# Kernel tuning notes

Hardware: AMD Instinct MI355X
Metric: run time of the kernel (lower is better)

The kernel has to match this reference:

```python
import jax, jax.numpy as jnp
import numpy as np

B, CIN, H, W = 32, 128, 64, 64
OUT, KH, KW = 256, 3, 3
NSK, SDIM = 4, 128


def setup_inputs() -> dict:
    key = jax.random.key(0)
    kx, kw_, kb, ks = jax.random.split(key, 4)
    x = jax.random.normal(kx, (B, CIN, H, W), dtype=jnp.float32)
    kval = float(np.sqrt(1.0 / (CIN * KH * KW)))  # groups=1
    weight = jax.random.uniform(kw_, (OUT, CIN, KH, KW), jnp.float32, -kval, kval)
    bias_tensor = jax.random.uniform(kb, (OUT,), jnp.float32, -kval, kval)
    # Rademacher / sketch_dim, shape (n, s, O) == torch's type1_signed_matrices
    signed = (2.0 * jax.random.bernoulli(ks, 0.5, (NSK, SDIM, OUT)).astype(jnp.float32) - 1.0) / SDIM
    # prod = einsum('ijkl,mi->mjkl') per sketch -> (n, s, Cin, kh, kw)
    prod = jnp.einsum('oikl,nso->nsikl', weight, signed)
    # .permute(2,3,1,0).flatten(0,2): (s,Cin,kh,kw) -> (kh,kw,Cin,s) -> (kh*kw*Cin, s)
    type1_sketches = prod.transpose(0, 3, 4, 2, 1).reshape(NSK, KH * KW * CIN, SDIM)
    return {
        "x": x,
        "type1_sketches": type1_sketches,
        "type1_signed_matrices": signed,
        "bias_tensor": bias_tensor,
    }


def reference(x, type1_sketches, type1_signed_matrices, bias_tensor):
    b, _, h1, w1 = x.shape
    h2 = h1 - KH + 1
    w2 = w1 - KW + 1
    # torch unfold: (B, Cin*KH*KW, E), features ordered channel-major (C, kh, kw)
    patches = jax.lax.conv_general_dilated_patches(
        x, filter_shape=(KH, KW), window_strides=(1, 1), padding='VALID'
    )  # (B, Cin*KH*KW, H2, W2)
    patches = patches.reshape(b, CIN * KH * KW, h2 * w2)  # (B, F, E)
    # 'bnfe,nfs->bnse' with the n-expansion folded away
    y = jnp.einsum('bfe,nfs->bnse', patches, type1_sketches)
    z = jnp.einsum('bnse,nso->bnoe', y, type1_signed_matrices)
    z = z.reshape(b, NSK, OUT, h2, w2)
    out = jnp.mean(z, axis=1) + bias_tensor[None, :, None, None]
    return out
```

## Files before the change

kernel.cpp:

```cpp
#include <hip/hip_runtime.h>
#include <hip/hip_bf16.h>
#include <stdint.h>


#define BATCH 32
#define CIN   128
#define HH    64
#define WW    64
#define OUTC  256
#define H2    62
#define W2    62
#define A_TILE 16384
#define WS_A_BYTES (36 * A_TILE)
#define BROWB 16384
#define AMAX  (35 * A_TILE)

typedef __bf16 bf16x8 __attribute__((ext_vector_type(8)));
typedef float  f32x4  __attribute__((ext_vector_type(4)));

typedef unsigned int u32_as1 __attribute__((address_space(1)));
typedef unsigned int u32_as3 __attribute__((address_space(3)));

__device__ __forceinline__ void async_copy16(const void* g, void* l) {
  __builtin_amdgcn_global_load_lds((const u32_as1*)g, (u32_as3*)l, 16, 0, 0);
}

#define FPB 4
__global__ __launch_bounds__(256) void weff_kernel(
    const float* __restrict__ sketches,
    const float* __restrict__ sgn,
    char* __restrict__ wsA)
{
  __shared__ alignas(16) float sk[512 * FPB];
  const int f0 = blockIdx.x * FPB;
  const int t  = threadIdx.x;

  for (int k = 0; k < (512 * FPB) / 256; ++k) {
    int idx = t + k * 256;
    int fi  = idx >> 9;
    int ns  = idx & 511;
    int n   = ns >> 7;
    int s   = ns & 127;
    sk[ns * FPB + fi] = sketches[(n * 1152 + f0 + fi) * 128 + s];
  }
  __syncthreads();

  const int o = t;
  float acc0 = 0.f, acc1 = 0.f, acc2 = 0.f, acc3 = 0.f;
#pragma unroll 8
  for (int ns = 0; ns < 512; ++ns) {
    float sg = sgn[ns * 256 + o];
    f32x4 skv = *(const f32x4*)(&sk[ns * FPB]);
    acc0 += sg * skv[0];
    acc1 += sg * skv[1];
    acc2 += sg * skv[2];
    acc3 += sg * skv[3];
  }

  float accs[FPB] = {acc0, acc1, acc2, acc3};
#pragma unroll
  for (int fi = 0; fi < FPB; ++fi) {
    int f   = f0 + fi;
    int c   = f / 9;
    int tap = f - c * 9;
    int st  = tap * 4 + (c >> 5);
    int kk  = c & 31;
    uint32_t byteoff = (uint32_t)st * A_TILE + (uint32_t)(o >> 4) * 1024
                     + (uint32_t)(((kk >> 3) * 16 + (o & 15)) * 16)
                     + (uint32_t)((kk & 7) * 2);
    *(__hip_bfloat16*)(wsA + byteoff) = __float2bfloat16(accs[fi] * 0.25f);
  }
}

__global__ __launch_bounds__(512, 2) void conv_kernel(
    const float* __restrict__ x,
    const char*  __restrict__ wA,
    const float* __restrict__ bias,
    float* __restrict__ out)
{
  __shared__ alignas(16) char lds[4 * A_TILE + 6 * BROWB];
  char* ldsA = lds;
  char* ldsB = lds + 4 * A_TILE;

  const int bid = blockIdx.x;
  const int swz = (bid & 7) * 64 + (bid >> 3);
  const int b   = swz >> 4;
  const int ig  = swz & 15;
  const int i0  = ig * 4;

  const int t    = threadIdx.x;
  const int lane = t & 63;
  const int w    = t >> 6;
  const int wm   = w >> 2;
  const int we   = w & 3;

  const char* aSrcLane = wA + w * 2048 + lane * 16;

#define STAGE(AOFF, TGT) do {                                              \
    const char* s_ = aSrcLane + (AOFF);                                    \
    char* d_ = ldsA + (TGT) * A_TILE + w * 2048;                           \
    async_copy16(s_,        d_);                                           \
    async_copy16(s_ + 1024, d_ + 1024);                                    \
  } while (0)

  STAGE(0, 0);
  STAGE(A_TILE, 1);
  STAGE(2 * A_TILE, 2);

  {
    const int j  = t & 63;
    const int cq = t >> 6;
    const uint32_t swb = (uint32_t)((j & 7) << 4);
#pragma unroll
    for (int r = 0; r < 6; ++r) {
      int xrow = i0 + r; if (xrow > 63) xrow = 63;
      const float* xr = x + (((size_t)(b * CIN + cq * 16)) * HH + xrow) * WW + j;
      char* lrow = ldsB + r * BROWB + j * 256;
#pragma unroll
      for (int g = 0; g < 2; ++g) {
        bf16x8 pk;
#pragma unroll
        for (int cc = 0; cc < 8; ++cc)
          pk[cc] = (__bf16)xr[(size_t)(g * 8 + cc) * (HH * WW)];
        uint32_t c0b = (uint32_t)(cq * 32 + g * 16);
        *(bf16x8*)(lrow + (c0b ^ swb)) = pk;
      }
    }
  }

  f32x4 acc[8][4];
  const f32x4 zf = {0.f, 0.f, 0.f, 0.f};
#pragma unroll
  for (int mi = 0; mi < 8; ++mi)
#pragma unroll
    for (int ni = 0; ni < 4; ++ni)
      acc[mi][ni] = zf;

  const int ln15  = lane & 15;
  const int khi16 = (lane >> 4) << 4;
  const char* pA = ldsA + wm * 8192 + lane * 16;

#define MKB(COL, PAR) (ldsB + we * BROWB + (COL) * 256                     \
    + (uint32_t)(((((PAR) * 64) | khi16) ^ (((COL) & 7) << 4))))
  const char* pB00 = MKB(ln15 + 0, 0); const char* pB01 = MKB(ln15 + 0, 1);
  const char* pB10 = MKB(ln15 + 1, 0); const char* pB11 = MKB(ln15 + 1, 1);
  const char* pB20 = MKB(ln15 + 2, 0); const char* pB21 = MKB(ln15 + 2, 1);
  const int c30 = (48 + ln15 + 0 > 63) ? 63 : 48 + ln15 + 0;
  const int c31 = (48 + ln15 + 1 > 63) ? 63 : 48 + ln15 + 1;
  const int c32 = (48 + ln15 + 2 > 63) ? 63 : 48 + ln15 + 2;
  const char* pC00 = MKB(c30, 0); const char* pC01 = MKB(c30, 1);
  const char* pC10 = MKB(c31, 0); const char* pC11 = MKB(c31, 1);
  const char* pC20 = MKB(c32, 0); const char* pC21 = MKB(c32, 1);
#undef MKB

  __syncthreads();

  bf16x8 aX0, aX1, aX2, aX3, aY0, aY1, aY2, aY3, b0, b1, b2, b3;

  aX0 = *(const bf16x8*)(pA);
  aX1 = *(const bf16x8*)(pA + 1024);
  aX2 = *(const bf16x8*)(pA + 2048);
  aX3 = *(const bf16x8*)(pA + 3072);
  b0  = *(const bf16x8*)(pB00);
  b1  = *(const bf16x8*)(pB00 + 4096);
  b2  = *(const bf16x8*)(pB00 + 8192);
  b3  = *(const bf16x8*)(pC00);

  uint32_t aoff = 3 * A_TILE;

#define MFMA_ __builtin_amdgcn_mfma_f32_16x16x32_bf16
#define LGKM0 asm volatile("s_waitcnt lgkmcnt(0)" ::: "memory")
#define VM2   asm volatile("s_waitcnt vmcnt(2)" ::: "memory")

#define MFMA16(A0_, A1_, A2_, A3_, M_) do {                                \
    __builtin_amdgcn_s_setprio(1);                                         \
    acc[(M_)+0][0] = MFMA_(A0_, b0, acc[(M_)+0][0], 0, 0, 0);              \
    acc[(M_)+0][1] = MFMA_(A0_, b1, acc[(M_)+0][1], 0, 0, 0);              \
    acc[(M_)+0][2] = MFMA_(A0_, b2, acc[(M_)+0][2], 0, 0, 0);              \
    acc[(M_)+0][3] = MFMA_(A0_, b3, acc[(M_)+0][3], 0, 0, 0);              \
    acc[(M_)+1][0] = MFMA_(A1_, b0, acc[(M_)+1][0], 0, 0, 0);              \
    acc[(M_)+1][1] = MFMA_(A1_, b1, acc[(M_)+1][1], 0, 0, 0);              \
    acc[(M_)+1][2] = MFMA_(A1_, b2, acc[(M_)+1][2], 0, 0, 0);              \
    acc[(M_)+1][3] = MFMA_(A1_, b3, acc[(M_)+1][3], 0, 0, 0);              \
    acc[(M_)+2][0] = MFMA_(A2_, b0, acc[(M_)+2][0], 0, 0, 0);              \
    acc[(M_)+2][1] = MFMA_(A2_, b1, acc[(M_)+2][1], 0, 0, 0);              \
    acc[(M_)+2][2] = MFMA_(A2_, b2, acc[(M_)+2][2], 0, 0, 0);              \
    acc[(M_)+2][3] = MFMA_(A2_, b3, acc[(M_)+2][3], 0, 0, 0);              \
    acc[(M_)+3][0] = MFMA_(A3_, b0, acc[(M_)+3][0], 0, 0, 0);              \
    acc[(M_)+3][1] = MFMA_(A3_, b1, acc[(M_)+3][1], 0, 0, 0);              \
    acc[(M_)+3][2] = MFMA_(A3_, b2, acc[(M_)+3][2], 0, 0, 0);              \
    acc[(M_)+3][3] = MFMA_(A3_, b3, acc[(M_)+3][3], 0, 0, 0);              \
    __builtin_amdgcn_s_setprio(0);                                         \
  } while (0)

#define STEPQ(Q, KWN, PARN, CK2N) do {                                     \
    VM2;                                                                   \
    __builtin_amdgcn_s_barrier();                                          \
    STAGE(aoff, (Q + 3) & 3);                                              \
    aoff += A_TILE; if (aoff > AMAX) aoff = AMAX;                          \
    LGKM0;                                                                 \
    MFMA16(aX0, aX1, aX2, aX3, 0);                                         \
    aY0 = *(const bf16x8*)(pA + (Q & 3) * A_TILE + 4096);                  \
    aY1 = *(const bf16x8*)(pA + (Q & 3) * A_TILE + 5120);                  \
    aY2 = *(const bf16x8*)(pA + (Q & 3) * A_TILE + 6144);                  \
    aY3 = *(const bf16x8*)(pA + (Q & 3) * A_TILE + 7168);                  \
    __builtin_amdgcn_s_barrier();                                          \
    LGKM0;                                                                 \
    MFMA16(aY0, aY1, aY2, aY3, 4);                                         \
    aX0 = *(const bf16x8*)(pA + ((Q + 1) & 3) * A_TILE);                   \
    aX1 = *(const bf16x8*)(pA + ((Q + 1) & 3) * A_TILE + 1024);            \
    aX2 = *(const bf16x8*)(pA + ((Q + 1) & 3) * A_TILE + 2048);            \
    aX3 = *(const bf16x8*)(pA + ((Q + 1) & 3) * A_TILE + 3072);            \
    b0 = *(const bf16x8*)(pB##KWN##PARN + (CK2N) * 128);                   \
    b1 = *(const bf16x8*)(pB##KWN##PARN + (CK2N) * 128 + 4096);            \
    b2 = *(const bf16x8*)(pB##KWN##PARN + (CK2N) * 128 + 8192);            \
    b3 = *(const bf16x8*)(pC##KWN##PARN + (CK2N) * 128);                   \
  } while (0)

#pragma unroll 1
  for (int kh = 0; kh < 3; ++kh) {
    STEPQ(0, 0, 1, 0);
    STEPQ(1, 0, 0, 1);
    STEPQ(2, 0, 1, 1);
    STEPQ(3, 1, 0, 0);
    STEPQ(4, 1, 1, 0);
    STEPQ(5, 1, 0, 1);
    STEPQ(6, 1, 1, 1);
    STEPQ(7, 2, 0, 0);
    STEPQ(8, 2, 1, 0);
    STEPQ(9, 2, 0, 1);
    STEPQ(10, 2, 1, 1);
    {
      VM2;
      __builtin_amdgcn_s_barrier();
      STAGE(aoff, (11 + 3) & 3);
      aoff += A_TILE; if (aoff > AMAX) aoff = AMAX;
      LGKM0;
      MFMA16(aX0, aX1, aX2, aX3, 0);
      aY0 = *(const bf16x8*)(pA + (11 & 3) * A_TILE + 4096);
      aY1 = *(const bf16x8*)(pA + (11 & 3) * A_TILE + 5120);
      aY2 = *(const bf16x8*)(pA + (11 & 3) * A_TILE + 6144);
      aY3 = *(const bf16x8*)(pA + (11 & 3) * A_TILE + 7168);
      __builtin_amdgcn_s_barrier();
      LGKM0;
      MFMA16(aY0, aY1, aY2, aY3, 4);
      if (kh < 2) {
        pB00 += BROWB; pB01 += BROWB; pB10 += BROWB; pB11 += BROWB;
        pB20 += BROWB; pB21 += BROWB; pC00 += BROWB; pC01 += BROWB;
        pC10 += BROWB; pC11 += BROWB; pC20 += BROWB; pC21 += BROWB;
      }
      aX0 = *(const bf16x8*)(pA);
      aX1 = *(const bf16x8*)(pA + 1024);
      aX2 = *(const bf16x8*)(pA + 2048);
      aX3 = *(const bf16x8*)(pA + 3072);
      b0 = *(const bf16x8*)(pB00);
      b1 = *(const bf16x8*)(pB00 + 4096);
      b2 = *(const bf16x8*)(pB00 + 8192);
      b3 = *(const bf16x8*)(pC00);
    }
  }

#undef STEPQ
#undef MFMA16
#undef VM2
#undef LGKM0
#undef MFMA_
#undef STAGE

  const int jn   = ln15;
  const int g4   = lane >> 4;
  const int irow = i0 + we;
  if (irow < H2) {
#pragma unroll
    for (int mi = 0; mi < 8; ++mi) {
#pragma unroll
      for (int ni = 0; ni < 4; ++ni) {
        const int jj = (ni << 4) + jn;
        if (jj < W2) {
#pragma unroll
          for (int rr = 0; rr < 4; ++rr) {
            const int o = (wm << 7) + (mi << 4) + (g4 << 2) + rr;
            out[(((size_t)b * OUTC + o) * H2 + irow) * W2 + jj] =
                acc[mi][ni][rr] + bias[o];
          }
        }
      }
    }
  }
}

extern "C" void kernel_launch(void* const* d_in, const int* in_sizes, int n_in,
                              void* d_out, int out_size, void* d_ws, size_t ws_size,
                              hipStream_t stream) {
  const float* x        = (const float*)d_in[0];
  const float* sketches = (const float*)d_in[1];
  const float* sgn      = (const float*)d_in[2];
  const float* bias     = (const float*)d_in[3];
  float* out            = (float*)d_out;
  char* wsA             = (char*)d_ws;

  if (ws_size < (size_t)WS_A_BYTES) return;

  weff_kernel<<<1152 / FPB, 256, 0, stream>>>(sketches, sgn, wsA);
  conv_kernel<<<BATCH * 16, 512, 0, stream>>>(x, wsA, bias, out);
}
```

Measured before the change: 105.3 us.

## Double-buffer B fragments in registers and drop the mid-step barrier

Splits the B operand registers into even and odd sets, so the next step's B fragments are read from LDS while the current step's MFMAs run. It also removes the second s_barrier and the explicit lgkmcnt(0) waits inside each step, leaving the compiler to insert the needed waits, with sched_barrier fences fixing the order of reads and MFMAs. The aim is to hide LDS read latency behind matrix math and cut synchronisation stalls. The cost is extra VGPR pressure, and it depends on the remaining per-step barrier being enough to keep the shared tile safe.

```diff
diff --git a/kernel.cpp b/kernel.cpp
--- a/kernel.cpp
+++ b/kernel.cpp
@@ -155,95 +155,93 @@
 
   __syncthreads();
 
-  bf16x8 aX0, aX1, aX2, aX3, aY0, aY1, aY2, aY3, b0, b1, b2, b3;
+  bf16x8 aX0, aX1, aX2, aX3, aY0, aY1, aY2, aY3;
+  bf16x8 bE0, bE1, bE2, bE3, bO0, bO1, bO2, bO3;
+
+#define READB(BN, KWN, PARN, CK2N) do {                                    \
+    BN##0 = *(const bf16x8*)(pB##KWN##PARN + (CK2N) * 128);                \
+    BN##1 = *(const bf16x8*)(pB##KWN##PARN + (CK2N) * 128 + 4096);         \
+    BN##2 = *(const bf16x8*)(pB##KWN##PARN + (CK2N) * 128 + 8192);         \
+    BN##3 = *(const bf16x8*)(pC##KWN##PARN + (CK2N) * 128);                \
+  } while (0)
 
   aX0 = *(const bf16x8*)(pA);
   aX1 = *(const bf16x8*)(pA + 1024);
   aX2 = *(const bf16x8*)(pA + 2048);
   aX3 = *(const bf16x8*)(pA + 3072);
-  b0  = *(const bf16x8*)(pB00);
-  b1  = *(const bf16x8*)(pB00 + 4096);
-  b2  = *(const bf16x8*)(pB00 + 8192);
-  b3  = *(const bf16x8*)(pC00);
+  READB(bE, 0, 0, 0);
 
   uint32_t aoff = 3 * A_TILE;
 
 #define MFMA_ __builtin_amdgcn_mfma_f32_16x16x32_bf16
-#define LGKM0 asm volatile("s_waitcnt lgkmcnt(0)" ::: "memory")
 #define VM2   asm volatile("s_waitcnt vmcnt(2)" ::: "memory")
-
-#define MFMA16(A0_, A1_, A2_, A3_, M_) do {                                \
+#define SB0   __builtin_amdgcn_sched_barrier(0)
+
+#define MFMA16(A0_, A1_, A2_, A3_, BS, M_) do {                            \
     __builtin_amdgcn_s_setprio(1);                                         \
-    acc[(M_)+0][0] = MFMA_(A0_, b0, acc[(M_)+0][0], 0, 0, 0);              \
-    acc[(M_)+0][1] = MFMA_(A0_, b1, acc[(M_)+0][1], 0, 0, 0);              \
-    acc[(M_)+0][2] = MFMA_(A0_, b2, acc[(M_)+0][2], 0, 0, 0);              \
-    acc[(M_)+0][3] = MFMA_(A0_, b3, acc[(M_)+0][3], 0, 0, 0);              \
-    acc[(M_)+1][0] = MFMA_(A1_, b0, acc[(M_)+1][0], 0, 0, 0);              \
-    acc[(M_)+1][1] = MFMA_(A1_, b1, acc[(M_)+1][1], 0, 0, 0);              \
-    acc[(M_)+1][2] = MFMA_(A1_, b2, acc[(M_)+1][2], 0, 0, 0);              \
-    acc[(M_)+1][3] = MFMA_(A1_, b3, acc[(M_)+1][3], 0, 0, 0);              \
-    acc[(M_)+2][0] = MFMA_(A2_, b0, acc[(M_)+2][0], 0, 0, 0);              \
-    acc[(M_)+2][1] = MFMA_(A2_, b1, acc[(M_)+2][1], 0, 0, 0);              \
-    acc[(M_)+2][2] = MFMA_(A2_, b2, acc[(M_)+2][2], 0, 0, 0);              \
-    acc[(M_)+2][3] = MFMA_(A2_, b3, acc[(M_)+2][3], 0, 0, 0);              \
-    acc[(M_)+3][0] = MFMA_(A3_, b0, acc[(M_)+3][0], 0, 0, 0);              \
-    acc[(M_)+3][1] = MFMA_(A3_, b1, acc[(M_)+3][1], 0, 0, 0);              \
-    acc[(M_)+3][2] = MFMA_(A3_, b2, acc[(M_)+3][2], 0, 0, 0);              \
-    acc[(M_)+3][3] = MFMA_(A3_, b3, acc[(M_)+3][3], 0, 0, 0);              \
+    acc[(M_)+0][0] = MFMA_(A0_, BS##0, acc[(M_)+0][0], 0, 0, 0);           \
+    acc[(M_)+0][1] = MFMA_(A0_, BS##1, acc[(M_)+0][1], 0, 0, 0);           \
+    acc[(M_)+0][2] = MFMA_(A0_, BS##2, acc[(M_)+0][2], 0, 0, 0);           \
+    acc[(M_)+0][3] = MFMA_(A0_, BS##3, acc[(M_)+0][3], 0, 0, 0);           \
+    acc[(M_)+1][0] = MFMA_(A1_, BS##0, acc[(M_)+1][0], 0, 0, 0);           \
+    acc[(M_)+1][1] = MFMA_(A1_, BS##1, acc[(M_)+1][1], 0, 0, 0);           \
+    acc[(M_)+1][2] = MFMA_(A1_, BS##2, acc[(M_)+1][2], 0, 0, 0);           \
+    acc[(M_)+1][3] = MFMA_(A1_, BS##3, acc[(M_)+1][3], 0, 0, 0);           \
+    acc[(M_)+2][0] = MFMA_(A2_, BS##0, acc[(M_)+2][0], 0, 0, 0);           \
+    acc[(M_)+2][1] = MFMA_(A2_, BS##1, acc[(M_)+2][1], 0, 0, 0);           \
+    acc[(M_)+2][2] = MFMA_(A2_, BS##2, acc[(M_)+2][2], 0, 0, 0);           \
+    acc[(M_)+2][3] = MFMA_(A2_, BS##3, acc[(M_)+2][3], 0, 0, 0);           \
+    acc[(M_)+3][0] = MFMA_(A3_, BS##0, acc[(M_)+3][0], 0, 0, 0);           \
+    acc[(M_)+3][1] = MFMA_(A3_, BS##1, acc[(M_)+3][1], 0, 0, 0);           \
+    acc[(M_)+3][2] = MFMA_(A3_, BS##2, acc[(M_)+3][2], 0, 0, 0);           \
+    acc[(M_)+3][3] = MFMA_(A3_, BS##3, acc[(M_)+3][3], 0, 0, 0);           \
     __builtin_amdgcn_s_setprio(0);                                         \
   } while (0)
 
-#define STEPQ(Q, KWN, PARN, CK2N) do {                                     \
+#define STEPQ(Q, BC, BN, KWN, PARN, CK2N) do {                             \
     VM2;                                                                   \
     __builtin_amdgcn_s_barrier();                                          \
     STAGE(aoff, (Q + 3) & 3);                                              \
     aoff += A_TILE; if (aoff > AMAX) aoff = AMAX;                          \
-    LGKM0;                                                                 \
-    MFMA16(aX0, aX1, aX2, aX3, 0);                                         \
     aY0 = *(const bf16x8*)(pA + (Q & 3) * A_TILE + 4096);                  \
     aY1 = *(const bf16x8*)(pA + (Q & 3) * A_TILE + 5120);                  \
     aY2 = *(const bf16x8*)(pA + (Q & 3) * A_TILE + 6144);                  \
     aY3 = *(const bf16x8*)(pA + (Q & 3) * A_TILE + 7168);                  \
-    __builtin_amdgcn_s_barrier();                                          \
-    LGKM0;                                                                 \
-    MFMA16(aY0, aY1, aY2, aY3, 4);                                         \
+    SB0;                                                                   \
+    MFMA16(aX0, aX1, aX2, aX3, BC, 0);                                     \
     aX0 = *(const bf16x8*)(pA + ((Q + 1) & 3) * A_TILE);                   \
     aX1 = *(const bf16x8*)(pA + ((Q + 1) & 3) * A_TILE + 1024);            \
     aX2 = *(const bf16x8*)(pA + ((Q + 1) & 3) * A_TILE + 2048);            \
     aX3 = *(const bf16x8*)(pA + ((Q + 1) & 3) * A_TILE + 3072);            \
-    b0 = *(const bf16x8*)(pB##KWN##PARN + (CK2N) * 128);                   \
-    b1 = *(const bf16x8*)(pB##KWN##PARN + (CK2N) * 128 + 4096);            \
-    b2 = *(const bf16x8*)(pB##KWN##PARN + (CK2N) * 128 + 8192);            \
-    b3 = *(const bf16x8*)(pC##KWN##PARN + (CK2N) * 128);                   \
+    READB(BN, KWN, PARN, CK2N);                                            \
+    SB0;                                                                   \
+    MFMA16(aY0, aY1, aY2, aY3, BC, 4);                                     \
   } while (0)
 
 #pragma unroll 1
   for (int kh = 0; kh < 3; ++kh) {
-    STEPQ(0, 0, 1, 0);
-    STEPQ(1, 0, 0, 1);
-    STEPQ(2, 0, 1, 1);
-    STEPQ(3, 1, 0, 0);
-    STEPQ(4, 1, 1, 0);
-    STEPQ(5, 1, 0, 1);
-    STEPQ(6, 1, 1, 1);
-    STEPQ(7, 2, 0, 0);
-    STEPQ(8, 2, 1, 0);
-    STEPQ(9, 2, 0, 1);
-    STEPQ(10, 2, 1, 1);
+    STEPQ(0,  bE, bO, 0, 1, 0);
+    STEPQ(1,  bO, bE, 0, 0, 1);
+    STEPQ(2,  bE, bO, 0, 1, 1);
+    STEPQ(3,  bO, bE, 1, 0, 0);
+    STEPQ(4,  bE, bO, 1, 1, 0);
+    STEPQ(5,  bO, bE, 1, 0, 1);
+    STEPQ(6,  bE, bO, 1, 1, 1);
+    STEPQ(7,  bO, bE, 2, 0, 0);
+    STEPQ(8,  bE, bO, 2, 1, 0);
+    STEPQ(9,  bO, bE, 2, 0, 1);
+    STEPQ(10, bE, bO, 2, 1, 1);
     {
       VM2;
       __builtin_amdgcn_s_barrier();
       STAGE(aoff, (11 + 3) & 3);
       aoff += A_TILE; if (aoff > AMAX) aoff = AMAX;
-      LGKM0;
-      MFMA16(aX0, aX1, aX2, aX3, 0);
       aY0 = *(const bf16x8*)(pA + (11 & 3) * A_TILE + 4096);
       aY1 = *(const bf16x8*)(pA + (11 & 3) * A_TILE + 5120);
       aY2 = *(const bf16x8*)(pA + (11 & 3) * A_TILE + 6144);
       aY3 = *(const bf16x8*)(pA + (11 & 3) * A_TILE + 7168);
-      __builtin_amdgcn_s_barrier();
-      LGKM0;
-      MFMA16(aY0, aY1, aY2, aY3, 4);
+      SB0;
+      MFMA16(aX0, aX1, aX2, aX3, bO, 0);
       if (kh < 2) {
         pB00 += BROWB; pB01 += BROWB; pB10 += BROWB; pB11 += BROWB;
         pB20 += BROWB; pB21 += BROWB; pC00 += BROWB; pC01 += BROWB;
@@ -253,18 +251,18 @@
       aX1 = *(const bf16x8*)(pA + 1024);
       aX2 = *(const bf16x8*)(pA + 2048);
       aX3 = *(const bf16x8*)(pA + 3072);
-      b0 = *(const bf16x8*)(pB00);
-      b1 = *(const bf16x8*)(pB00 + 4096);
-      b2 = *(const bf16x8*)(pB00 + 8192);
-      b3 = *(const bf16x8*)(pC00);
+      READB(bE, 0, 0, 0);
+      SB0;
+      MFMA16(aY0, aY1, aY2, aY3, bO, 4);
     }
   }
 
 #undef STEPQ
 #undef MFMA16
+#undef SB0
 #undef VM2
-#undef LGKM0
 #undef MFMA_
+#undef READB
 #undef STAGE
 
   const int jn   = ln15;
```

Measured after the change: 107.1 us. No clear change (+1.7%).

## Restructure main loop into ping-pong style with extra barriers and no register prefetch

Applied to the files above, without the earlier changes.

Each step now issues its own LDS fragment loads for A-low and B plus the next global stage, then waits with a looser vmcnt. Two half-steps of 16 MFMAs each are bracketed by workgroup barriers and sched_barrier fences. This removes the cross-iteration register prefetch in favor of barrier-coordinated phases, likely aiming for ping-pong interleaving between waves. The risk is that fragment loads are no longer overlapped with the previous MFMA block, and the extra barriers add stalls.

```diff
diff --git a/kernel.cpp b/kernel.cpp
--- a/kernel.cpp
+++ b/kernel.cpp
@@ -155,22 +155,13 @@
 
   __syncthreads();
 
-  bf16x8 aX0, aX1, aX2, aX3, aY0, aY1, aY2, aY3, b0, b1, b2, b3;
-
-  aX0 = *(const bf16x8*)(pA);
-  aX1 = *(const bf16x8*)(pA + 1024);
-  aX2 = *(const bf16x8*)(pA + 2048);
-  aX3 = *(const bf16x8*)(pA + 3072);
-  b0  = *(const bf16x8*)(pB00);
-  b1  = *(const bf16x8*)(pB00 + 4096);
-  b2  = *(const bf16x8*)(pB00 + 8192);
-  b3  = *(const bf16x8*)(pC00);
-
+  bf16x8 aL0, aL1, aL2, aL3, aH0, aH1, aH2, aH3, b0, b1, b2, b3;
   uint32_t aoff = 3 * A_TILE;
 
 #define MFMA_ __builtin_amdgcn_mfma_f32_16x16x32_bf16
+#define VM4   asm volatile("s_waitcnt vmcnt(4)" ::: "memory")
 #define LGKM0 asm volatile("s_waitcnt lgkmcnt(0)" ::: "memory")
-#define VM2   asm volatile("s_waitcnt vmcnt(2)" ::: "memory")
+#define SB0   __builtin_amdgcn_sched_barrier(0)
 
 #define MFMA16(A0_, A1_, A2_, A3_, M_) do {                                \
     __builtin_amdgcn_s_setprio(1);                                         \
@@ -193,77 +184,58 @@
     __builtin_amdgcn_s_setprio(0);                                         \
   } while (0)
 
-#define STEPQ(Q, KWN, PARN, CK2N) do {                                     \
-    VM2;                                                                   \
-    __builtin_amdgcn_s_barrier();                                          \
+#define STEPQ(Q, KW, PAR, CK2) do {                                        \
+    aL0 = *(const bf16x8*)(pA + (Q & 3) * A_TILE);                         \
+    aL1 = *(const bf16x8*)(pA + (Q & 3) * A_TILE + 1024);                  \
+    aL2 = *(const bf16x8*)(pA + (Q & 3) * A_TILE + 2048);                  \
+    aL3 = *(const bf16x8*)(pA + (Q & 3) * A_TILE + 3072);                  \
+    b0 = *(const bf16x8*)(pB##KW##PAR + (CK2) * 128);                      \
+    b1 = *(const bf16x8*)(pB##KW##PAR + (CK2) * 128 + 4096);               \
+    b2 = *(const bf16x8*)(pB##KW##PAR + (CK2) * 128 + 8192);               \
+    b3 = *(const bf16x8*)(pC##KW##PAR + (CK2) * 128);                      \
     STAGE(aoff, (Q + 3) & 3);                                              \
     aoff += A_TILE; if (aoff > AMAX) aoff = AMAX;                          \
-    LGKM0;                                                                 \
-    MFMA16(aX0, aX1, aX2, aX3, 0);                                         \
-    aY0 = *(const bf16x8*)(pA + (Q & 3) * A_TILE + 4096);                  \
-    aY1 = *(const bf16x8*)(pA + (Q & 3) * A_TILE + 5120);                  \
-    aY2 = *(const bf16x8*)(pA + (Q & 3) * A_TILE + 6144);                  \
-    aY3 = *(const bf16x8*)(pA + (Q & 3) * A_TILE + 7168);                  \
-    __builtin_amdgcn_s_barrier();                                          \
-    LGKM0;                                                                 \
-    MFMA16(aY0, aY1, aY2, aY3, 4);                                         \
-    aX0 = *(const bf16x8*)(pA + ((Q + 1) & 3) * A_TILE);                   \
-    aX1 = *(const bf16x8*)(pA + ((Q + 1) & 3) * A_TILE + 1024);            \
-    aX2 = *(const bf16x8*)(pA + ((Q + 1) & 3) * A_TILE + 2048);            \
-    aX3 = *(const bf16x8*)(pA + ((Q + 1) & 3) * A_TILE + 3072);            \
-    b0 = *(const bf16x8*)(pB##KWN##PARN + (CK2N) * 128);                   \
-    b1 = *(const bf16x8*)(pB##KWN##PARN + (CK2N) * 128 + 4096);            \
-    b2 = *(const bf16x8*)(pB##KWN##PARN + (CK2N) * 128 + 8192);            \
-    b3 = *(const bf16x8*)(pC##KWN##PARN + (CK2N) * 128);                   \
+    VM4;                                                                   \
+    __builtin_amdgcn_s_barrier();                                          \
+    LGKM0; SB0;                                                            \
+    MFMA16(aL0, aL1, aL2, aL3, 0);                                         \
+    __builtin_amdgcn_s_barrier();                                          \
+    aH0 = *(const bf16x8*)(pA + (Q & 3) * A_TILE + 4096);                  \
+    aH1 = *(const bf16x8*)(pA + (Q & 3) * A_TILE + 5120);                  \
+    aH2 = *(const bf16x8*)(pA + (Q & 3) * A_TILE + 6144);                  \
+    aH3 = *(const bf16x8*)(pA + (Q & 3) * A_TILE + 7168);                  \
+    __builtin_amdgcn_s_barrier();                                          \
+    LGKM0; SB0;                                                            \
+    MFMA16(aH0, aH1, aH2, aH3, 4);                                         \
+    __builtin_amdgcn_s_barrier();                                          \
   } while (0)
 
 #pragma unroll 1
   for (int kh = 0; kh < 3; ++kh) {
-    STEPQ(0, 0, 1, 0);
-    STEPQ(1, 0, 0, 1);
-    STEPQ(2, 0, 1, 1);
-    STEPQ(3, 1, 0, 0);
-    STEPQ(4, 1, 1, 0);
-    STEPQ(5, 1, 0, 1);
-    STEPQ(6, 1, 1, 1);
-    STEPQ(7, 2, 0, 0);
-    STEPQ(8, 2, 1, 0);
-    STEPQ(9, 2, 0, 1);
-    STEPQ(10, 2, 1, 1);
-    {
-      VM2;
-      __builtin_amdgcn_s_barrier();
-      STAGE(aoff, (11 + 3) & 3);
-      aoff += A_TILE; if (aoff > AMAX) aoff = AMAX;
-      LGKM0;
-      MFMA16(aX0, aX1, aX2, aX3, 0);
-      aY0 = *(const bf16x8*)(pA + (11 & 3) * A_TILE + 4096);
-      aY1 = *(const bf16x8*)(pA + (11 & 3) * A_TILE + 5120);
-      aY2 = *(const bf16x8*)(pA + (11 & 3) * A_TILE + 6144);
-      aY3 = *(const bf16x8*)(pA + (11 & 3) * A_TILE + 7168);
-      __builtin_amdgcn_s_barrier();
-      LGKM0;
-      MFMA16(aY0, aY1, aY2, aY3, 4);
-      if (kh < 2) {
-        pB00 += BROWB; pB01 += BROWB; pB10 += BROWB; pB11 += BROWB;
-        pB20 += BROWB; pB21 += BROWB; pC00 += BROWB; pC01 += BROWB;
-        pC10 += BROWB; pC11 += BROWB; pC20 += BROWB; pC21 += BROWB;
-      }
-      aX0 = *(const bf16x8*)(pA);
-      aX1 = *(const bf16x8*)(pA + 1024);
-      aX2 = *(const bf16x8*)(pA + 2048);
-      aX3 = *(const bf16x8*)(pA + 3072);
-      b0 = *(const bf16x8*)(pB00);
-      b1 = *(const bf16x8*)(pB00 + 4096);
-      b2 = *(const bf16x8*)(pB00 + 8192);
-      b3 = *(const bf16x8*)(pC00);
+    STEPQ(0,  0, 0, 0);
+    STEPQ(1,  0, 1, 0);
+    STEPQ(2,  0, 0, 1);
+    STEPQ(3,  0, 1, 1);
+    STEPQ(4,  1, 0, 0);
+    STEPQ(5,  1, 1, 0);
+    STEPQ(6,  1, 0, 1);
+    STEPQ(7,  1, 1, 1);
+    STEPQ(8,  2, 0, 0);
+    STEPQ(9,  2, 1, 0);
+    STEPQ(10, 2, 0, 1);
+    STEPQ(11, 2, 1, 1);
+    if (kh < 2) {
+      pB00 += BROWB; pB01 += BROWB; pB10 += BROWB; pB11 += BROWB;
+      pB20 += BROWB; pB21 += BROWB; pC00 += BROWB; pC01 += BROWB;
+      pC10 += BROWB; pC11 += BROWB; pC20 += BROWB; pC21 += BROWB;
     }
   }
 
 #undef STEPQ
 #undef MFMA16
-#undef VM2
+#undef SB0
 #undef LGKM0
+#undef VM4
 #undef MFMA_
 #undef STAGE
 
```

New measurement: 109.9 us. 1.04x slower.
